# Kernel optimization log

Hardware: AMD Instinct MI355X
Metric: run time of the kernel (lower is better)

The kernel has to match this reference:

```python
import jax, jax.numpy as jnp
import numpy as np

B, S, SE = 4, 1024, 1024
E, H, M = 768, 12, 100
D = E // H
EPS = 1e-5
GELU_C = 0.7978845608028654  # sqrt(2/pi)


def _ln(x, g, b):
    mu = x.mean(-1, keepdims=True)
    v = ((x - mu) ** 2).mean(-1, keepdims=True)
    return g * (x - mu) / jnp.sqrt(v + EPS) + b


def _gelu(x):
    return 0.5 * x * (1.0 + jnp.tanh(GELU_C * (x + 0.044715 * x ** 3)))


def _split(x):  # [b,s,E] -> [b,H,s,D]
    b, s, _ = x.shape
    return x.reshape(b, s, H, D).transpose(0, 2, 1, 3)


def _merge(x):  # [b,H,s,D] -> [b,s,E]
    b, h, s, d = x.shape
    return x.transpose(0, 2, 1, 3).reshape(b, s, h * d)


def _forward(x, encoder_features, ln1_g, ln1_b, ln2_g, ln2_b,
             c_attn_w, c_attn_b, attn_proj_w, attn_proj_b,
             memory_features, mem_attn_w, mem_attn_b, mem_alpha_w, mem_alpha_b,
             fcq_w, fcq_b, fck_w, fck_b, fcv_w, fcv_b, enc_proj_w, enc_proj_b,
             fc_alpha1_w, fc_alpha1_b, fc_alpha2_w, fc_alpha2_b,
             mlp_fc_w, mlp_fc_b, mlp_proj_w, mlp_proj_b, mask_encoder):
    # ---- memory-augmented self-attention (note: original has NO 1/sqrt(d) scaling here) ----
    h = _ln(x, ln1_g, ln1_b)
    qkv = h @ c_attn_w + c_attn_b
    q, k, v = jnp.split(qkv, 3, axis=-1)
    q, k, v = _split(q), _split(k), _split(v)
    w = jax.nn.softmax(jnp.einsum('bhqd,bhkd->bhqk', q, k), axis=-1)
    a = _merge(jnp.einsum('bhqk,bhkd->bhqd', w, v))
    # memory slots are batch-independent -> compute once, broadcast over batch
    mem = memory_features[0] @ mem_attn_w + mem_attn_b  # [M, 2E]
    mk, mv = jnp.split(mem, 2, axis=-1)
    mk = mk.reshape(M, H, D).transpose(1, 2, 0)  # [H,D,M]
    mv = mv.reshape(M, H, D).transpose(1, 0, 2)  # [H,M,D]
    wm = jax.nn.softmax(jnp.einsum('bhqd,hdm->bhqm', q, mk), axis=-1)
    a1 = _merge(jnp.einsum('bhqm,hmd->bhqd', wm, mv))
    al = jax.nn.sigmoid(jnp.concatenate([a, a1], -1) @ mem_alpha_w + mem_alpha_b)
    a = al * a + (1.0 - al) * a1
    a = a @ attn_proj_w + attn_proj_b
    a = x + a  # residual (dropout = identity in eval)

    # ---- two cross-attentions sharing weights and ln_1 ----
    ha = _ln(a, ln1_g, ln1_b)

    def enc_dec(enc):
        qe = _split(ha @ fcq_w + fcq_b)
        ke = _split(enc @ fck_w + fck_b)
        ve = _split(enc @ fcv_w + fcv_b)
        we = jnp.einsum('bhqd,bhkd->bhqk', qe, ke) / np.float32(np.sqrt(D))
        we = jnp.where(mask_encoder, jnp.float32(-10000.0), we)
        we = jax.nn.softmax(we, axis=-1)
        o = _merge(jnp.einsum('bhqk,bhkd->bhqd', we, ve))
        return o @ enc_proj_w + enc_proj_b

    e1 = enc_dec(_ln(encoder_features[:, 0], ln1_g, ln1_b))
    e2 = enc_dec(_ln(encoder_features[:, 1], ln1_g, ln1_b))
    al1 = jax.nn.sigmoid(jnp.concatenate([a, e1], -1) @ fc_alpha1_w + fc_alpha1_b)
    al2 = jax.nn.sigmoid(jnp.concatenate([a, e2], -1) @ fc_alpha2_w + fc_alpha2_b)
    e1 = al1 * a + (1.0 - al1) * e1
    e2 = al2 * a + (1.0 - al2) * e2
    a = (e1 + e2) / np.float32(np.sqrt(2.0))

    # ---- MLP ----
    hm = _ln(a, ln2_g, ln2_b)
    m = _gelu(hm @ mlp_fc_w + mlp_fc_b) @ mlp_proj_w + mlp_proj_b
    return a + m


def setup_inputs() -> dict:
    key = jax.random.key(0)
    ks = iter(jax.random.split(key, 48))

    def rn(shape, s=0.02):
        return jax.random.normal(next(ks), shape, jnp.float32) * s

    return dict(
        x=jax.random.normal(next(ks), (B, S, E), jnp.float32),
        encoder_features=jax.random.normal(next(ks), (B, 2, SE, E), jnp.float32),
        mask_encoder=jax.random.bernoulli(next(ks), 0.1, (B, 1, 1, SE)),
        ln1_g=jnp.ones(E, jnp.float32), ln1_b=jnp.zeros(E, jnp.float32),
        ln2_g=jnp.ones(E, jnp.float32), ln2_b=jnp.zeros(E, jnp.float32),
        c_attn_w=rn((E, 3 * E)), c_attn_b=jnp.zeros(3 * E, jnp.float32),
        attn_proj_w=rn((E, E)), attn_proj_b=jnp.zeros(E, jnp.float32),
        memory_features=rn((1, M, E), 1.0),
        mem_attn_w=rn((E, 2 * E)), mem_attn_b=jnp.zeros(2 * E, jnp.float32),
        mem_alpha_w=rn((2 * E, E)), mem_alpha_b=jnp.zeros(E, jnp.float32),
        fcq_w=rn((E, E)), fcq_b=jnp.zeros(E, jnp.float32),
        fck_w=rn((E, E)), fck_b=jnp.zeros(E, jnp.float32),
        fcv_w=rn((E, E)), fcv_b=jnp.zeros(E, jnp.float32),
        enc_proj_w=rn((E, E)), enc_proj_b=jnp.zeros(E, jnp.float32),
        fc_alpha1_w=rn((2 * E, E)), fc_alpha1_b=jnp.zeros(E, jnp.float32),
        fc_alpha2_w=rn((2 * E, E)), fc_alpha2_b=jnp.zeros(E, jnp.float32),
        mlp_fc_w=rn((E, 4 * E)), mlp_fc_b=jnp.zeros(4 * E, jnp.float32),
        mlp_proj_w=rn((4 * E, E)), mlp_proj_b=jnp.zeros(E, jnp.float32),
    )


def reference(x, encoder_features, mask_encoder, ln1_g, ln1_b, ln2_g, ln2_b,
              c_attn_w, c_attn_b, attn_proj_w, attn_proj_b,
              memory_features, mem_attn_w, mem_attn_b, mem_alpha_w, mem_alpha_b,
              fcq_w, fcq_b, fck_w, fck_b, fcv_w, fcv_b, enc_proj_w, enc_proj_b,
              fc_alpha1_w, fc_alpha1_b, fc_alpha2_w, fc_alpha2_b,
              mlp_fc_w, mlp_fc_b, mlp_proj_w, mlp_proj_b):
    return _forward(x, encoder_features, ln1_g, ln1_b, ln2_g, ln2_b,
                    c_attn_w, c_attn_b, attn_proj_w, attn_proj_b,
                    memory_features, mem_attn_w, mem_attn_b, mem_alpha_w, mem_alpha_b,
                    fcq_w, fcq_b, fck_w, fck_b, fcv_w, fcv_b, enc_proj_w, enc_proj_b,
                    fc_alpha1_w, fc_alpha1_b, fc_alpha2_w, fc_alpha2_b,
                    mlp_fc_w, mlp_fc_b, mlp_proj_w, mlp_proj_b, mask_encoder)
```

## Files before the change

kernel.cpp:

```cpp
#include <hip/hip_runtime.h>

typedef __bf16 bf16_t;
typedef __bf16 bf16x8v __attribute__((ext_vector_type(8)));
typedef float f32x4 __attribute__((ext_vector_type(4)));

#define CB 4
#define CE 768
#define CH 12
#define CD 64

__device__ __forceinline__ float fexp2(float x) { return __builtin_amdgcn_exp2f(x); }

__device__ __forceinline__ void gload16(const void* g, void* l) {
    __builtin_amdgcn_global_load_lds((const __attribute__((address_space(1))) void*)g,
                                     (__attribute__((address_space(3))) void*)l, 16, 0, 0);
}

__device__ __forceinline__ void xcd_remap(int& bx, int& by, int gx, int gy) {
    int nwg = gx * gy;
    if ((nwg & 7) == 0) {
        int lin = by * gx + bx;
        int lin2 = (lin & 7) * (nwg >> 3) + (lin >> 3);
        bx = lin2 % gx;
        by = lin2 / gx;
    }
}

template<int BM, int BN, int CONCAT, int ACT, int RES, int OUT, int CMODE>
__global__ __launch_bounds__(256)
void gemm_n(const bf16_t* __restrict__ A0, const bf16_t* __restrict__ A1,
            const bf16_t* __restrict__ Bt, const float* __restrict__ bias,
            const float* __restrict__ bias2, const void* __restrict__ resid,
            void* __restrict__ C, void* __restrict__ C2, void* __restrict__ C3,
            int M, int N, int K, int lda, int ldc)
{
    constexpr int WM = BM / 2, WN = BN / 2, RM = WM / 16, RN = WN / 16;
    __shared__ __align__(16) bf16_t As0[BM * 64], As1[BM * 64];
    __shared__ __align__(16) bf16_t Bs0[BN * 64], Bs1[BN * 64];

    const int t = threadIdx.x;
    const int lane = t & 63, wave = t >> 6;
    int bx = blockIdx.x, by = blockIdx.y;
    xcd_remap(bx, by, gridDim.x, gridDim.y);
    const int m0 = by * BM, n0 = bx * BN;
    const int wm = (wave & 1) * WM, wn = (wave >> 1) * WN;
    const int fr = lane & 15, quad = lane >> 4;

    const int lr = lane >> 3;
    const int kof = ((lane & 7) ^ lr) * 8;

    const bf16_t* A1b = A1;
    if (CMODE == 6) A1b = A1 + (n0 >= 768 ? (long)4096 * 768 : 0);

    f32x4 acc[RM][RN];
#pragma unroll
    for (int i = 0; i < RM; i++)
#pragma unroll
        for (int j = 0; j < RN; j++)
#pragma unroll
            for (int p = 0; p < 4; p++) acc[i][j][p] = 0.f;

    auto stage = [&](bf16_t* As, bf16_t* Bs, int kt) {
        const bf16_t* Ab = A0;
        int kk = kt;
        if (CONCAT && kt >= 768) { Ab = A1b; kk = kt - 768; }
        const bf16_t* asrc = Ab + (long)(m0 + wave * 8 + lr) * lda + kk + kof;
#pragma unroll
        for (int c = 0; c < BM / 32; ++c)
            gload16(asrc + (long)c * 32 * lda, &As[(c * 32 + wave * 8) * 64]);
        const bf16_t* bsrc = Bt + (long)(n0 + wave * 8 + lr) * K + kt + kof;
#pragma unroll
        for (int c = 0; c < BN / 32; ++c)
            gload16(bsrc + (long)c * 32 * K, &Bs[(c * 32 + wave * 8) * 64]);
    };

    const int sw = fr & 7;
    auto compute = [&](const bf16_t* As, const bf16_t* Bs) {
        bf16x8v af[RM][2], bfr[RN][2];
        const int s0 = quad ^ sw;
#pragma unroll
        for (int i = 0; i < RM; ++i) {
            const char* rb = (const char*)As + (wm + i * 16 + fr) * 128;
            af[i][0] = *(const bf16x8v*)(rb + (s0 << 4));
            af[i][1] = *(const bf16x8v*)(rb + ((s0 ^ 4) << 4));
        }
#pragma unroll
        for (int j = 0; j < RN; ++j) {
            const char* rb = (const char*)Bs + (wn + j * 16 + fr) * 128;
            bfr[j][0] = *(const bf16x8v*)(rb + (s0 << 4));
            bfr[j][1] = *(const bf16x8v*)(rb + ((s0 ^ 4) << 4));
        }
#pragma unroll
        for (int ks = 0; ks < 2; ++ks)
#pragma unroll
            for (int i = 0; i < RM; ++i)
#pragma unroll
                for (int j = 0; j < RN; ++j)
                    acc[i][j] = __builtin_amdgcn_mfma_f32_16x16x32_bf16(af[i][ks], bfr[j][ks], acc[i][j], 0, 0, 0);
    };

    const int nk = K >> 6;
    stage(As0, Bs0, 0);
    __syncthreads();
    for (int kt = 0; kt + 2 <= nk; kt += 2) {
        stage(As1, Bs1, (kt + 1) << 6);
        compute(As0, Bs0);
        __syncthreads();
        if (kt + 2 < nk) stage(As0, Bs0, (kt + 2) << 6);
        compute(As1, Bs1);
        __syncthreads();
    }

    const int rq = quad * 4, cn = fr;
#pragma unroll
    for (int i = 0; i < RM; i++)
#pragma unroll
        for (int j = 0; j < RN; j++) {
            int col = n0 + wn + j * 16 + cn;
            int t3 = (CMODE == 4 || CMODE == 5) ? (col / 768) : 0;
            int cc = col - t3 * 768;
            float bv = 0.f;
            if (CMODE == 5)      bv = t3 ? bias2[cc] : bias[cc];
            else if (CMODE == 6) bv = (col < 768) ? bias[col] : bias2[col - 768];
            else if (bias)       bv = bias[col];
            const int row0 = m0 + wm + i * 16 + rq;
            float vv[4];
#pragma unroll
            for (int p = 0; p < 4; p++) {
                float v = acc[i][j][p] + bv;
                if (ACT == 1) v = 1.f / (1.f + __expf(-v));
                if (ACT == 2) {
                    float u2 = 1.5957691216057308f * (v + 0.044715f * v * v * v);
                    v = v / (1.f + __expf(-u2));
                }
                if (RES == 2) v += ((const float*)resid)[(long)(row0 + p) * ldc + col];
                vv[p] = v;
            }
            if (CMODE == 0) {
#pragma unroll
                for (int p = 0; p < 4; p++) {
                    long idx = (long)(row0 + p) * ldc + col;
                    if (OUT == 0)      ((bf16_t*)C)[idx] = (bf16_t)vv[p];
                    else if (OUT == 1) ((float*)C)[idx] = vv[p];
                    else { ((float*)C)[idx] = vv[p]; ((bf16_t*)C2)[idx] = (bf16_t)vv[p]; }
                }
            } else if (CMODE == 6) {
                long base = (col < 768) ? 0 : ((long)4096 * 768 - 768);
#pragma unroll
                for (int p = 0; p < 4; p++)
                    ((bf16_t*)C)[base + (long)(row0 + p) * 768 + col] = (bf16_t)vv[p];
            } else {
                int bb = row0 >> 10, ss0 = row0 & 1023;
                int hh = cc >> 6, dd = cc & 63;
                long srow = (long)(bb * CH + hh) * 1024 + ss0;
                long tbase = (((long)(bb * CH + hh) * 64) + dd) * 1024 + ss0;
                union { ushort4 u4; bf16_t b[4]; } pk;
#pragma unroll
                for (int p = 0; p < 4; p++) pk.b[p] = (bf16_t)vv[p];
                if (CMODE == 2) {
#pragma unroll
                    for (int p = 0; p < 4; p++)
                        ((bf16_t*)C)[(srow + p) * 64 + dd] = pk.b[p];
                } else if (CMODE == 5) {
                    if (t3 == 0) {
#pragma unroll
                        for (int p = 0; p < 4; p++)
                            ((bf16_t*)C)[(srow + p) * 64 + dd] = pk.b[p];
                    } else {
                        *(ushort4*)((bf16_t*)C2 + tbase) = pk.u4;
                    }
                } else {
                    if (t3 == 0) {
#pragma unroll
                        for (int p = 0; p < 4; p++)
                            ((bf16_t*)C)[(srow + p) * 64 + dd] = pk.b[p];
                    } else if (t3 == 1) {
#pragma unroll
                        for (int p = 0; p < 4; p++)
                            ((bf16_t*)C2)[(srow + p) * 64 + dd] = pk.b[p];
                    } else {
                        *(ushort4*)((bf16_t*)C3 + tbase) = pk.u4;
                    }
                }
            }
        }
}

template<int MODE>
__global__ __launch_bounds__(256)
void flash_attn(const bf16_t* __restrict__ Q, const bf16_t* __restrict__ K,
                const bf16_t* __restrict__ V, const int* __restrict__ mask,
                bf16_t* __restrict__ O)
{
    __shared__ __align__(16) bf16_t Qs[64 * 72];
    __shared__ __align__(16) bf16_t Ks0[64 * 64], Ks1[64 * 64];
    __shared__ __align__(16) bf16_t Vs[64 * 64];

    const int t = threadIdx.x;
    const int lane = t & 63, wave = t >> 6;
    int bx = blockIdx.x, bz = blockIdx.z;
    {
        int nwg = gridDim.x * gridDim.z;
        if ((nwg & 7) == 0) {
            int lin = bz * gridDim.x + bx;
            int lin2 = (lin & 7) * (nwg >> 3) + (lin >> 3);
            bx = lin2 % gridDim.x;
            bz = lin2 / gridDim.x;
        }
    }
    const int zq = (MODE == 1) ? (bz % 48) : bz;
    const int b = zq / CH, h = bz % CH;
    const long eoff = (MODE == 1) ? (long)(bz / 48) * ((long)4096 * 768) : 0;
    const int q0 = bx * 64;

    const bf16_t* Qb = Q + (long)zq * 65536 + (long)q0 * 64;
    const bf16_t* Kb = (MODE == 2) ? K + (long)h * (128 * 64) : K + (long)bz * 65536;
    const bf16_t* Vb = (MODE == 2) ? V + (long)h * (64 * 128) : V + (long)bz * 65536;
    const int ldv = (MODE == 2) ? 128 : 1024;
    const int NT = (MODE == 2) ? 2 : 16;
    constexpr float SCL = (MODE == 1) ? 0.18033688011112042f : 1.4426950408889634f;

    const int lr = lane >> 3, kof = ((lane & 7) ^ lr) * 8;

    auto stageK = [&](bf16_t* Ks, int kt) {
#pragma unroll
        for (int c = 0; c < 2; ++c) {
            int r = wave * 8 + c * 32;
            gload16(Kb + (long)(kt * 64 + r + lr) * 64 + kof, &Ks[r * 64]);
        }
    };
    auto stageV = [&](int kt) {
#pragma unroll
        for (int c = 0; c < 2; ++c) {
            int r = wave * 8 + c * 32;
            gload16(Vb + (long)(r + lr) * ldv + kt * 64 + kof, &Vs[r * 64]);
        }
    };

    stageK(Ks0, 0);
    const int r0 = t >> 3, c0 = (t & 7) * 8;
    for (int rr = r0; rr < 64; rr += 32)
        *(uint4*)&Qs[rr * 72 + c0] = *(const uint4*)&Qb[(long)rr * 64 + c0];
    __syncthreads();

    const int fr = lane & 15, quad = lane >> 4;
    const int sw = fr & 7;
    bf16x8v qf[2];
#pragma unroll
    for (int ks = 0; ks < 2; ks++)
        qf[ks] = *(const bf16x8v*)&Qs[(wave * 16 + fr) * 72 + quad * 8 + ks * 32];

    bf16_t* Ps = &Qs[wave * 16 * 72];

    f32x4 o[4];
    float mrow[4], lrow[4];
#pragma unroll
    for (int p = 0; p < 4; p++) { mrow[p] = -1e30f; lrow[p] = 0.f; }
#pragma unroll
    for (int j = 0; j < 4; j++)
#pragma unroll
        for (int p = 0; p < 4; p++) o[j][p] = 0.f;

    auto qkt_sm = [&](const bf16_t* Ks, int kt) {
        f32x4 s[4];
#pragma unroll
        for (int j = 0; j < 4; j++)
#pragma unroll
            for (int p = 0; p < 4; p++) s[j][p] = 0.f;
#pragma unroll
        for (int ks = 0; ks < 2; ks++) {
            bf16x8v bk[4];
#pragma unroll
            for (int j = 0; j < 4; j++) {
                const char* rb = (const char*)Ks + (j * 16 + fr) * 128;
                bk[j] = *(const bf16x8v*)(rb + (((quad ^ sw) ^ (ks << 2)) << 4));
            }
#pragma unroll
            for (int j = 0; j < 4; j++)
                s[j] = __builtin_amdgcn_mfma_f32_16x16x32_bf16(qf[ks], bk[j], s[j], 0, 0, 0);
        }
        if (MODE == 1) {
#pragma unroll
            for (int j = 0; j < 4; j++) {
                int mv = mask[(long)b * 1024 + kt * 64 + j * 16 + fr];
#pragma unroll
                for (int p = 0; p < 4; p++)
                    s[j][p] = mv ? -14426.95f : s[j][p] * SCL;
            }
        } else {
#pragma unroll
            for (int j = 0; j < 4; j++)
#pragma unroll
                for (int p = 0; p < 4; p++) {
                    s[j][p] *= SCL;
                    if (MODE == 2 && kt * 64 + j * 16 + fr >= 100) s[j][p] = -1e30f;
                }
        }
        float tmax[4];
        bool need = false;
#pragma unroll
        for (int p = 0; p < 4; p++) {
            float tm = fmaxf(fmaxf(s[0][p], s[1][p]), fmaxf(s[2][p], s[3][p]));
            tm = fmaxf(tm, __shfl_xor(tm, 1, 64));
            tm = fmaxf(tm, __shfl_xor(tm, 2, 64));
            tm = fmaxf(tm, __shfl_xor(tm, 4, 64));
            tm = fmaxf(tm, __shfl_xor(tm, 8, 64));
            tmax[p] = tm;
            need = need || (tm > mrow[p] + 8.f);
        }
        if (__any(need ? 1 : 0)) {
#pragma unroll
            for (int p = 0; p < 4; p++) {
                float mnew = fmaxf(mrow[p], tmax[p]);
                float alpha = fexp2(mrow[p] - mnew);
                lrow[p] *= alpha;
#pragma unroll
                for (int j = 0; j < 4; j++) o[j][p] *= alpha;
                mrow[p] = mnew;
            }
        }
#pragma unroll
        for (int p = 0; p < 4; p++) {
            float rs = 0.f;
#pragma unroll
            for (int j = 0; j < 4; j++) {
                float e = fexp2(s[j][p] - mrow[p]);
                s[j][p] = e;
                rs += e;
            }
            rs += __shfl_xor(rs, 1, 64);
            rs += __shfl_xor(rs, 2, 64);
            rs += __shfl_xor(rs, 4, 64);
            rs += __shfl_xor(rs, 8, 64);
            lrow[p] += rs;
        }
#pragma unroll
        for (int j = 0; j < 4; j++)
#pragma unroll
            for (int p = 0; p < 4; p++)
                Ps[(quad * 4 + p) * 72 + j * 16 + fr] = (bf16_t)s[j][p];
    };

    auto pv = [&]() {
#pragma unroll
        for (int ks = 0; ks < 2; ks++) {
            bf16x8v af = *(const bf16x8v*)&Ps[fr * 72 + quad * 8 + ks * 32];
            bf16x8v bv[4];
#pragma unroll
            for (int j = 0; j < 4; j++) {
                const char* rb = (const char*)Vs + (j * 16 + fr) * 128;
                bv[j] = *(const bf16x8v*)(rb + (((quad ^ sw) ^ (ks << 2)) << 4));
            }
#pragma unroll
            for (int j = 0; j < 4; j++)
                o[j] = __builtin_amdgcn_mfma_f32_16x16x32_bf16(af, bv[j], o[j], 0, 0, 0);
        }
    };

    for (int kt = 0; kt < NT; kt += 2) {
        stageV(kt);
        if (kt + 1 < NT) stageK(Ks1, kt + 1);
        qkt_sm(Ks0, kt);
        __syncthreads();
        pv();
        __syncthreads();
        stageV(kt + 1);
        if (kt + 2 < NT) stageK(Ks0, kt + 2);
        qkt_sm(Ks1, kt + 1);
        __syncthreads();
        pv();
        __syncthreads();
    }
#pragma unroll
    for (int p = 0; p < 4; p++) {
        float inv = 1.f / lrow[p];
        int srow = q0 + wave * 16 + quad * 4 + p;
        long base = ((long)b * 1024 + srow) * 768 + h * 64 + eoff;
#pragma unroll
        for (int j = 0; j < 4; j++)
            O[base + j * 16 + fr] = (bf16_t)(o[j][p] * inv);
    }
}

__device__ __forceinline__ void ln_body(const float* in, bf16_t* out,
                                        const float* g, const float* b,
                                        long base, long ob, int t)
{
    __shared__ float red[4];
    float v0 = in[base + t], v1 = in[base + t + 256], v2 = in[base + t + 512];
    float s = v0 + v1 + v2;
    for (int m = 32; m; m >>= 1) s += __shfl_xor(s, m, 64);
    if ((t & 63) == 0) red[t >> 6] = s;
    __syncthreads();
    s = red[0] + red[1] + red[2] + red[3];
    __syncthreads();
    const float mu = s * (1.f / 768.f);
    float d0 = v0 - mu, d1 = v1 - mu, d2 = v2 - mu;
    float q = d0 * d0 + d1 * d1 + d2 * d2;
    for (int m = 32; m; m >>= 1) q += __shfl_xor(q, m, 64);
    if ((t & 63) == 0) red[t >> 6] = q;
    __syncthreads();
    q = red[0] + red[1] + red[2] + red[3];
    const float rstd = rsqrtf(q * (1.f / 768.f) + 1e-5f);
    out[ob + t]       = (bf16_t)(g[t]       * d0 * rstd + b[t]);
    out[ob + t + 256] = (bf16_t)(g[t + 256] * d1 * rstd + b[t + 256]);
    out[ob + t + 512] = (bf16_t)(g[t + 512] * d2 * rstd + b[t + 512]);
}

__global__ __launch_bounds__(256)
void ln_kernel(const float* __restrict__ in, bf16_t* __restrict__ out,
               const float* __restrict__ g, const float* __restrict__ b)
{
    const int r = blockIdx.x;
    ln_body(in, out, g, b, (long)r * CE, (long)r * CE, threadIdx.x);
}

__global__ __launch_bounds__(256)
void ln_enc(const float* __restrict__ encf, bf16_t* __restrict__ out,
            const float* __restrict__ g, const float* __restrict__ b)
{
    const int r = blockIdx.x;
    const int e = r >> 12, rr = r & 4095, bb = rr >> 10, s = rr & 1023;
    ln_body(encf, out, g, b, ((long)(bb * 2 + e) * 1024 + s) * CE, (long)r * CE, threadIdx.x);
}

__global__ void blend_kernel(const bf16_t* __restrict__ al, bf16_t* __restrict__ a,
                             const bf16_t* __restrict__ a1)
{
    int idx = blockIdx.x * 256 + threadIdx.x;
    float g = (float)al[idx];
    a[idx] = (bf16_t)(g * (float)a[idx] + (1.f - g) * (float)a1[idx]);
}

__global__ void fuse_gates2(const bf16_t* __restrict__ gal, const bf16_t* __restrict__ eo,
                            float* __restrict__ rf)
{
    const long SZel = (long)4096 * 768;
    long idx = (long)blockIdx.x * 256 + threadIdx.x;
    float g1 = (float)gal[idx], g2 = (float)gal[idx + SZel];
    float e1 = (float)eo[idx],  e2 = (float)eo[idx + SZel];
    float r = rf[idx];
    float v = g1 * r + (1.f - g1) * e1 + g2 * r + (1.f - g2) * e2;
    rf[idx] = v * 0.7071067811865476f;
}

__global__ void zero_out(float* __restrict__ out)
{
    out[blockIdx.x * 256 + threadIdx.x] = 0.f;
}

__global__ void transpose_cast(const float* __restrict__ in, bf16_t* __restrict__ out,
                               int K, int N)
{
    __shared__ bf16_t tile[32][33];
    int n0 = blockIdx.x * 32, k0 = blockIdx.y * 32;
    int tx = threadIdx.x, ty = threadIdx.y;
    for (int i = ty; i < 32; i += 8)
        tile[i][tx] = (bf16_t)in[(long)(k0 + i) * N + n0 + tx];
    __syncthreads();
    for (int i = ty; i < 32; i += 8)
        out[(long)(n0 + i) * K + k0 + tx] = tile[tx][i];
}

__global__ void cast_pad_mem(const float* __restrict__ memf, bf16_t* __restrict__ out)
{
    int idx = blockIdx.x * 256 + threadIdx.x;
    int row = idx / 768;
    out[idx] = (row < 100) ? (bf16_t)memf[idx] : (bf16_t)0.f;
}

__global__ void repack_mem(const bf16_t* __restrict__ mem, bf16_t* __restrict__ mkt,
                           bf16_t* __restrict__ mvt)
{
    int idx = blockIdx.x * 256 + threadIdx.x;
    int d = idx & 63;
    int slot = (idx >> 6) & 127;
    int h = idx >> 13;
    bf16_t kv = (slot < 100) ? mem[slot * 1536 + h * CD + d] : (bf16_t)0.f;
    bf16_t vv = (slot < 100) ? mem[slot * 1536 + CE + h * CD + d] : (bf16_t)0.f;
    mkt[idx] = kv;
    mvt[((long)h * 64 + d) * 128 + slot] = vv;
}

extern "C" void kernel_launch(void* const* d_in, const int* in_sizes, int n_in,
                              void* d_out, int out_size, void* d_ws, size_t ws_size,
                              hipStream_t stream)
{
    (void)in_sizes; (void)n_in; (void)out_size;
    const float* x        = (const float*)d_in[0];
    const float* encf     = (const float*)d_in[1];
    const int*   maskenc  = (const int*)d_in[2];
    const float* ln1_g    = (const float*)d_in[3];
    const float* ln1_b    = (const float*)d_in[4];
    const float* ln2_g    = (const float*)d_in[5];
    const float* ln2_b    = (const float*)d_in[6];
    const float* c_attn_w = (const float*)d_in[7];
    const float* c_attn_b = (const float*)d_in[8];
    const float* aproj_w  = (const float*)d_in[9];
    const float* aproj_b  = (const float*)d_in[10];
    const float* memf     = (const float*)d_in[11];
    const float* mattn_w  = (const float*)d_in[12];
    const float* mattn_b  = (const float*)d_in[13];
    const float* malpha_w = (const float*)d_in[14];
    const float* malpha_b = (const float*)d_in[15];
    const float* fcq_w    = (const float*)d_in[16];
    const float* fcq_b    = (const float*)d_in[17];
    const float* fck_w    = (const float*)d_in[18];
    const float* fck_b    = (const float*)d_in[19];
    const float* fcv_w    = (const float*)d_in[20];
    const float* fcv_b    = (const float*)d_in[21];
    const float* eproj_w  = (const float*)d_in[22];
    const float* eproj_b  = (const float*)d_in[23];
    const float* fa1_w    = (const float*)d_in[24];
    const float* fa1_b    = (const float*)d_in[25];
    const float* fa2_w    = (const float*)d_in[26];
    const float* fa2_b    = (const float*)d_in[27];
    const float* mfc_w    = (const float*)d_in[28];
    const float* mfc_b    = (const float*)d_in[29];
    const float* mproj_w  = (const float*)d_in[30];
    const float* mproj_b  = (const float*)d_in[31];
    float* dout = (float*)d_out;

    size_t off = 0;
    auto alloc = [&](size_t bytes) -> void* {
        void* p = (char*)d_ws + off;
        off = (off + bytes + 255) & ~(size_t)255;
        return p;
    };
    const size_t SZ = (size_t)4096 * 768 * 2;
    const long SZel = (long)4096 * 768;
    bf16_t* wt_cattn  = (bf16_t*)alloc((size_t)2304 * 768 * 2);
    bf16_t* wt_aproj  = (bf16_t*)alloc((size_t)768 * 768 * 2);
    bf16_t* wt_malpha = (bf16_t*)alloc((size_t)768 * 1536 * 2);
    bf16_t* wt_fcq    = (bf16_t*)alloc((size_t)768 * 768 * 2);
    bf16_t* wt_fck    = (bf16_t*)alloc((size_t)768 * 768 * 2);
    bf16_t* wt_fcv    = (bf16_t*)alloc((size_t)768 * 768 * 2);
    bf16_t* wt_eproj  = (bf16_t*)alloc((size_t)768 * 768 * 2);
    bf16_t* wt_fa1    = (bf16_t*)alloc((size_t)768 * 1536 * 2);
    bf16_t* wt_fa2    = (bf16_t*)alloc((size_t)768 * 1536 * 2);
    bf16_t* wt_mfc    = (bf16_t*)alloc((size_t)3072 * 768 * 2);
    bf16_t* wt_mproj  = (bf16_t*)alloc((size_t)768 * 3072 * 2);
    bf16_t* wt_mattn  = (bf16_t*)alloc((size_t)1536 * 768 * 2);
    bf16_t* memb   = (bf16_t*)alloc((size_t)128 * 768 * 2);
    bf16_t* membuf = (bf16_t*)alloc((size_t)128 * 1536 * 2);
    bf16_t* mkt    = (bf16_t*)alloc((size_t)CH * 128 * 64 * 2);
    bf16_t* mvt    = (bf16_t*)alloc((size_t)CH * 64 * 128 * 2);
    bf16_t* bufA   = (bf16_t*)alloc(SZ);
    bf16_t* qbuf   = (bf16_t*)alloc(SZ);
    bf16_t* kbuf   = (bf16_t*)alloc(2 * SZ);
    bf16_t* vtbuf  = (bf16_t*)alloc(2 * SZ);
    bf16_t* asbuf  = (bf16_t*)alloc(2 * SZ);
    bf16_t* bufB   = (bf16_t*)alloc(2 * SZ);
    float*  residf = (float*)alloc((size_t)4096 * 768 * 4);
    bf16_t* residb = (bf16_t*)alloc(SZ);

    if (off > ws_size) {
        zero_out<<<12288, 256, 0, stream>>>(dout);
        return;
    }
    bf16_t* mid = kbuf;
    bf16_t* galbuf = kbuf;
    bf16_t* eobuf = bufB;

    const dim3 blk(256);

    auto T = [&](const float* w, bf16_t* wt, int Kd, int Nd) {
        transpose_cast<<<dim3(Nd / 32, Kd / 32), dim3(32, 8), 0, stream>>>(w, wt, Kd, Nd);
    };
    T(c_attn_w, wt_cattn, 768, 2304);
    T(aproj_w, wt_aproj, 768, 768);
    T(malpha_w, wt_malpha, 1536, 768);
    T(fcq_w, wt_fcq, 768, 768);
    T(fck_w, wt_fck, 768, 768);
    T(fcv_w, wt_fcv, 768, 768);
    T(eproj_w, wt_eproj, 768, 768);
    T(fa1_w, wt_fa1, 1536, 768);
    T(fa2_w, wt_fa2, 1536, 768);
    T(mfc_w, wt_mfc, 768, 3072);
    T(mproj_w, wt_mproj, 3072, 768);
    T(mattn_w, wt_mattn, 768, 1536);

    cast_pad_mem<<<384, blk, 0, stream>>>(memf, memb);
    gemm_n<64,64,0,0,0,0,0><<<dim3(24, 2), blk, 0, stream>>>(
        memb, nullptr, wt_mattn, mattn_b, nullptr, nullptr, membuf, nullptr, nullptr,
        128, 1536, 768, 768, 1536);
    repack_mem<<<384, blk, 0, stream>>>(membuf, mkt, mvt);

    ln_kernel<<<4096, blk, 0, stream>>>(x, bufA, ln1_g, ln1_b);
    gemm_n<128,128,0,0,0,0,4><<<dim3(18, 32), blk, 0, stream>>>(
        bufA, nullptr, wt_cattn, c_attn_b, nullptr, nullptr, qbuf, kbuf, vtbuf,
        4096, 2304, 768, 768, 0);

    flash_attn<0><<<dim3(16, 1, 48), blk, 0, stream>>>(qbuf, kbuf, vtbuf, nullptr, asbuf);
    flash_attn<2><<<dim3(16, 1, 48), blk, 0, stream>>>(qbuf, mkt, mvt, nullptr, asbuf + SZel);

    gemm_n<128,64,1,1,0,0,0><<<dim3(12, 32), blk, 0, stream>>>(
        asbuf, asbuf + SZel, wt_malpha, malpha_b, nullptr, nullptr, bufA, nullptr, nullptr,
        4096, 768, 1536, 768, 768);
    blend_kernel<<<12288, blk, 0, stream>>>(bufA, asbuf, asbuf + SZel);
    gemm_n<128,64,0,0,2,2,0><<<dim3(12, 32), blk, 0, stream>>>(
        asbuf, nullptr, wt_aproj, aproj_b, nullptr, x, residf, residb, nullptr,
        4096, 768, 768, 768, 768);

    ln_kernel<<<4096, blk, 0, stream>>>(residf, bufA, ln1_g, ln1_b);
    gemm_n<128,64,0,0,0,0,2><<<dim3(12, 32), blk, 0, stream>>>(
        bufA, nullptr, wt_fcq, fcq_b, nullptr, nullptr, qbuf, nullptr, nullptr,
        4096, 768, 768, 768, 0);

    ln_enc<<<8192, blk, 0, stream>>>(encf, bufB, ln1_g, ln1_b);
    gemm_n<128,128,0,0,0,0,5><<<dim3(12, 64), blk, 0, stream>>>(
        bufB, nullptr, wt_fck, fck_b, fcv_b, nullptr, kbuf, vtbuf, nullptr,
        8192, 1536, 768, 768, 0);
    flash_attn<1><<<dim3(16, 1, 96), blk, 0, stream>>>(
        qbuf, kbuf, vtbuf, maskenc, asbuf);
    gemm_n<128,128,0,0,0,0,0><<<dim3(6, 64), blk, 0, stream>>>(
        asbuf, nullptr, wt_eproj, eproj_b, nullptr, nullptr, eobuf, nullptr, nullptr,
        8192, 768, 768, 768, 768);
    gemm_n<128,64,1,1,0,0,6><<<dim3(24, 32), blk, 0, stream>>>(
        residb, eobuf, wt_fa1, fa1_b, fa2_b, nullptr, galbuf, nullptr, nullptr,
        4096, 1536, 1536, 768, 768);
    fuse_gates2<<<12288, blk, 0, stream>>>(galbuf, eobuf, residf);

    ln_kernel<<<4096, blk, 0, stream>>>(residf, bufA, ln2_g, ln2_b);
    gemm_n<128,128,0,2,0,0,0><<<dim3(24, 32), blk, 0, stream>>>(
        bufA, nullptr, wt_mfc, mfc_b, nullptr, nullptr, mid, nullptr, nullptr,
        4096, 3072, 768, 768, 3072);
    gemm_n<128,64,0,0,2,1,0><<<dim3(12, 32), blk, 0, stream>>>(
        mid, nullptr, wt_mproj, mproj_b, nullptr, residf, dout, nullptr, nullptr,
        4096, 768, 3072, 3072, 768);
}
```

Baseline: 651.0 us.

## Transpose QK^T MFMA output so each lane owns one query row in softmax

Swaps the MFMA operands so the score tile comes out transposed, letting each lane hold a single query row. Row max and row sum then need two cross-quad shuffles instead of four per row, and the running max and sum shrink to scalars. The softmax scale is folded into Q once in bf16, the mask is read as int4 vectors, and P is stored with packed 8-byte writes. MFMA sections are also wrapped in s_setprio raises; pre-scaling Q in bf16 adds a small rounding change, and per-row alpha and normalizer values must now be redistributed by shuffle.

```diff
diff --git a/kernel.cpp b/kernel.cpp
--- a/kernel.cpp
+++ b/kernel.cpp
@@ -247,15 +247,16 @@
     const int sw = fr & 7;
     bf16x8v qf[2];
 #pragma unroll
-    for (int ks = 0; ks < 2; ks++)
-        qf[ks] = *(const bf16x8v*)&Qs[(wave * 16 + fr) * 72 + quad * 8 + ks * 32];
+    for (int ks = 0; ks < 2; ks++) {
+        bf16x8v raw = *(const bf16x8v*)&Qs[(wave * 16 + fr) * 72 + quad * 8 + ks * 32];
+#pragma unroll
+        for (int i = 0; i < 8; i++) qf[ks][i] = (bf16_t)((float)raw[i] * SCL);
+    }
 
     bf16_t* Ps = &Qs[wave * 16 * 72];
 
     f32x4 o[4];
-    float mrow[4], lrow[4];
-#pragma unroll
-    for (int p = 0; p < 4; p++) { mrow[p] = -1e30f; lrow[p] = 0.f; }
+    float mrow = -1e30f, lrow = 0.f;
 #pragma unroll
     for (int j = 0; j < 4; j++)
 #pragma unroll
@@ -267,6 +268,7 @@
         for (int j = 0; j < 4; j++)
 #pragma unroll
             for (int p = 0; p < 4; p++) s[j][p] = 0.f;
+        __builtin_amdgcn_s_setprio(1);
 #pragma unroll
         for (int ks = 0; ks < 2; ks++) {
             bf16x8v bk[4];
@@ -277,71 +279,71 @@
             }
 #pragma unroll
             for (int j = 0; j < 4; j++)
-                s[j] = __builtin_amdgcn_mfma_f32_16x16x32_bf16(qf[ks], bk[j], s[j], 0, 0, 0);
-        }
+                s[j] = __builtin_amdgcn_mfma_f32_16x16x32_bf16(bk[j], qf[ks], s[j], 0, 0, 0);
+        }
+        __builtin_amdgcn_s_setprio(0);
         if (MODE == 1) {
 #pragma unroll
             for (int j = 0; j < 4; j++) {
-                int mv = mask[(long)b * 1024 + kt * 64 + j * 16 + fr];
+                int4 mv = *(const int4*)&mask[(long)b * 1024 + kt * 64 + j * 16 + quad * 4];
+                s[j][0] = mv.x ? -14426.95f : s[j][0];
+                s[j][1] = mv.y ? -14426.95f : s[j][1];
+                s[j][2] = mv.z ? -14426.95f : s[j][2];
+                s[j][3] = mv.w ? -14426.95f : s[j][3];
+            }
+        }
+        if (MODE == 2) {
+#pragma unroll
+            for (int j = 0; j < 4; j++)
 #pragma unroll
                 for (int p = 0; p < 4; p++)
-                    s[j][p] = mv ? -14426.95f : s[j][p] * SCL;
-            }
-        } else {
+                    if (kt * 64 + j * 16 + quad * 4 + p >= 100) s[j][p] = -1e30f;
+        }
+        float tm = s[0][0];
+#pragma unroll
+        for (int j = 0; j < 4; j++)
+#pragma unroll
+            for (int p = 0; p < 4; p++) tm = fmaxf(tm, s[j][p]);
+        tm = fmaxf(tm, __shfl_xor(tm, 16, 64));
+        tm = fmaxf(tm, __shfl_xor(tm, 32, 64));
+        bool need = tm > mrow + 8.f;
+        if (__any(need ? 1 : 0)) {
+            float mnew = fmaxf(mrow, tm);
+            float alpha = fexp2(mrow - mnew);
+            lrow *= alpha;
+            mrow = mnew;
+            float arow[4];
+#pragma unroll
+            for (int p = 0; p < 4; p++)
+                arow[p] = __shfl(alpha, (lane & 48) | (quad * 4 + p), 64);
 #pragma unroll
             for (int j = 0; j < 4; j++)
 #pragma unroll
-                for (int p = 0; p < 4; p++) {
-                    s[j][p] *= SCL;
-                    if (MODE == 2 && kt * 64 + j * 16 + fr >= 100) s[j][p] = -1e30f;
-                }
-        }
-        float tmax[4];
-        bool need = false;
-#pragma unroll
-        for (int p = 0; p < 4; p++) {
-            float tm = fmaxf(fmaxf(s[0][p], s[1][p]), fmaxf(s[2][p], s[3][p]));
-            tm = fmaxf(tm, __shfl_xor(tm, 1, 64));
-            tm = fmaxf(tm, __shfl_xor(tm, 2, 64));
-            tm = fmaxf(tm, __shfl_xor(tm, 4, 64));
-            tm = fmaxf(tm, __shfl_xor(tm, 8, 64));
-            tmax[p] = tm;
-            need = need || (tm > mrow[p] + 8.f);
-        }
-        if (__any(need ? 1 : 0)) {
+                for (int p = 0; p < 4; p++) o[j][p] *= arow[p];
+        }
+        float rs = 0.f;
+#pragma unroll
+        for (int j = 0; j < 4; j++)
 #pragma unroll
             for (int p = 0; p < 4; p++) {
-                float mnew = fmaxf(mrow[p], tmax[p]);
-                float alpha = fexp2(mrow[p] - mnew);
-                lrow[p] *= alpha;
-#pragma unroll
-                for (int j = 0; j < 4; j++) o[j][p] *= alpha;
-                mrow[p] = mnew;
-            }
-        }
-#pragma unroll
-        for (int p = 0; p < 4; p++) {
-            float rs = 0.f;
-#pragma unroll
-            for (int j = 0; j < 4; j++) {
-                float e = fexp2(s[j][p] - mrow[p]);
+                float e = fexp2(s[j][p] - mrow);
                 s[j][p] = e;
                 rs += e;
             }
-            rs += __shfl_xor(rs, 1, 64);
-            rs += __shfl_xor(rs, 2, 64);
-            rs += __shfl_xor(rs, 4, 64);
-            rs += __shfl_xor(rs, 8, 64);
-            lrow[p] += rs;
-        }
-#pragma unroll
-        for (int j = 0; j < 4; j++)
-#pragma unroll
-            for (int p = 0; p < 4; p++)
-                Ps[(quad * 4 + p) * 72 + j * 16 + fr] = (bf16_t)s[j][p];
+        rs += __shfl_xor(rs, 16, 64);
+        rs += __shfl_xor(rs, 32, 64);
+        lrow += rs;
+#pragma unroll
+        for (int j = 0; j < 4; j++) {
+            union { uint2 u; bf16_t bb[4]; } pk;
+#pragma unroll
+            for (int p = 0; p < 4; p++) pk.bb[p] = (bf16_t)s[j][p];
+            *(uint2*)&Ps[fr * 72 + j * 16 + quad * 4] = pk.u;
+        }
     };
 
     auto pv = [&]() {
+        __builtin_amdgcn_s_setprio(1);
 #pragma unroll
         for (int ks = 0; ks < 2; ks++) {
             bf16x8v af = *(const bf16x8v*)&Ps[fr * 72 + quad * 8 + ks * 32];
@@ -355,6 +357,7 @@
             for (int j = 0; j < 4; j++)
                 o[j] = __builtin_amdgcn_mfma_f32_16x16x32_bf16(af, bv[j], o[j], 0, 0, 0);
         }
+        __builtin_amdgcn_s_setprio(0);
     };
 
     for (int kt = 0; kt < NT; kt += 2) {
@@ -371,14 +374,17 @@
         pv();
         __syncthreads();
     }
+    float linv[4];
+#pragma unroll
+    for (int p = 0; p < 4; p++)
+        linv[p] = 1.f / __shfl(lrow, (lane & 48) | (quad * 4 + p), 64);
 #pragma unroll
     for (int p = 0; p < 4; p++) {
-        float inv = 1.f / lrow[p];
         int srow = q0 + wave * 16 + quad * 4 + p;
         long base = ((long)b * 1024 + srow) * 768 + h * 64 + eoff;
 #pragma unroll
         for (int j = 0; j < 4; j++)
-            O[base + j * 16 + fr] = (bf16_t)(o[j][p] * inv);
+            O[base + j * 16 + fr] = (bf16_t)(o[j][p] * linv[p]);
     }
 }
 
```

Measured after the change: 600.5 us. -7.8%, faster.
